# Performance work log

Hardware: AMD Instinct MI355X
Metric: run time of the kernel (lower is better)

## Reference

```python
import jax, jax.numpy as jnp
import numpy as np

B, IN, H = 8192, 1024, 1024

def setup_inputs() -> dict:
    key = jax.random.key(0)
    ks = jax.random.split(key, 7)
    s_in = 1.0 / np.sqrt(IN)
    s_h = 1.0 / np.sqrt(H)
    return {
        "x": jax.random.normal(ks[0], (B, IN), jnp.float32),
        "h": jax.random.normal(ks[1], (B, H), jnp.float32),
        "c": jax.random.normal(ks[2], (B, H), jnp.float32),
        "Wx": jax.random.normal(ks[3], (4, H, IN), jnp.float32) * s_in,
        "bx": jax.random.normal(ks[4], (4, H), jnp.float32) * s_in,
        "Wh": jax.random.normal(ks[5], (4, H, H), jnp.float32) * s_h,
        "bh": jax.random.normal(ks[6], (4, H), jnp.float32) * s_h,
    }

def reference(x, h, c, Wx, bx, Wh, bh):
    # gate order along axis g: 0=i (input), 1=f (forget), 2=g (cell), 3=o (output)
    # two fused GEMMs over all 4 gates: [B,4,H]
    gates = (jnp.einsum('bi,goi->bgo', x, Wx)
             + jnp.einsum('bj,goj->bgo', h, Wh)
             + bx[None] + bh[None])
    i = jax.nn.sigmoid(gates[:, 0])
    f = jax.nn.sigmoid(gates[:, 1])
    g = jnp.tanh(gates[:, 2])
    o = jax.nn.sigmoid(gates[:, 3])
    c_next = f * c + i * g
    h_next = o * jnp.tanh(c_next)
    return (h_next, c_next)
```

## Files before the change

kernel.cpp:

```cpp
#include <hip/hip_runtime.h>
#include <hip/hip_bf16.h>
#include <cstdint>
#include <cstddef>


#define B_DIM   8192
#define IN_DIM  1024
#define H_DIM   1024
#define KTOT    2048
#define BK      64
#define KSTEPS  (KTOT / BK)

typedef __attribute__((ext_vector_type(8))) short  bf16x8;
typedef __attribute__((ext_vector_type(4))) float  f32x4;

__device__ __forceinline__ void gld_lds16(const void* g, void* l) {
    __builtin_amdgcn_global_load_lds(
        (const __attribute__((address_space(1))) void*)g,
        (__attribute__((address_space(3))) void*)l, 16, 0, 0);
}

__device__ __forceinline__ unsigned short f2bf(float f) {
    union { float f; unsigned u; } v; v.f = f;
    unsigned r = v.u + 0x7fffu + ((v.u >> 16) & 1u);
    return (unsigned short)(r >> 16);
}

__global__ __launch_bounds__(256) void pack_a(const float* __restrict__ x,
                                              const float* __restrict__ h,
                                              unsigned short* __restrict__ Acat) {
    int idx = blockIdx.x * 256 + threadIdx.x;
    int row = idx >> 8;
    int k0  = (idx & 255) * 8;
    const float* src = (k0 < IN_DIM) ? (x + (size_t)row * IN_DIM + k0)
                                     : (h + (size_t)row * H_DIM + (k0 - IN_DIM));
    f32x4 v0 = *(const f32x4*)src;
    f32x4 v1 = *(const f32x4*)(src + 4);
    unsigned short tmp[8];
#pragma unroll
    for (int j = 0; j < 4; ++j) tmp[j]     = f2bf(v0[j]);
#pragma unroll
    for (int j = 0; j < 4; ++j) tmp[4 + j] = f2bf(v1[j]);
    *(bf16x8*)(Acat + (size_t)idx * 8) = *(const bf16x8*)tmp;
}

__global__ __launch_bounds__(256) void pack_w(const float* __restrict__ Wx,
                                              const float* __restrict__ Wh,
                                              unsigned short* __restrict__ Wcat) {
    int idx = blockIdx.x * 256 + threadIdx.x;
    int n   = idx >> 8;
    int k0  = (idx & 255) * 8;
    int ob = n >> 7, g = (n >> 5) & 3, ol = n & 31;
    int o  = ob * 32 + ol;
    const float* src = (k0 < IN_DIM)
        ? (Wx + ((size_t)(g * H_DIM + o)) * IN_DIM + k0)
        : (Wh + ((size_t)(g * H_DIM + o)) * H_DIM + (k0 - IN_DIM));
    f32x4 v0 = *(const f32x4*)src;
    f32x4 v1 = *(const f32x4*)(src + 4);
    unsigned short tmp[8];
#pragma unroll
    for (int j = 0; j < 4; ++j) tmp[j]     = f2bf(v0[j]);
#pragma unroll
    for (int j = 0; j < 4; ++j) tmp[4 + j] = f2bf(v1[j]);
    *(bf16x8*)(Wcat + (size_t)idx * 8) = *(const bf16x8*)tmp;
}

__device__ __forceinline__ float sigmoidf_fast(float v) {
    return 1.0f / (1.0f + __expf(-v));
}

__global__ __launch_bounds__(256, 2) void lstm_gemm(
        const unsigned short* __restrict__ Acat,
        const unsigned short* __restrict__ Wcat,
        const float* __restrict__ c,
        const float* __restrict__ bx,
        const float* __restrict__ bh,
        float* __restrict__ outH,
        float* __restrict__ outC) {
    __shared__ __align__(16) char smem[32768];
    char* ldsA = smem;
    char* ldsB = smem + 16384;

    const int t    = threadIdx.x;
    const int lane = t & 63;
    const int wid  = t >> 6;
    const int nb   = blockIdx.x;
    const int mb   = blockIdx.y;
    const int m0   = mb * 128;
    const int n0r  = nb * 128;
    const int l15  = lane & 15;
    const int l4   = lane >> 4;

    f32x4 acc[2][8];
#pragma unroll
    for (int i = 0; i < 2; ++i)
#pragma unroll
        for (int j = 0; j < 8; ++j)
#pragma unroll
            for (int e = 0; e < 4; ++e) acc[i][j][e] = 0.0f;

    const char* Abase = (const char*)Acat;
    const char* Wbase = (const char*)Wcat;

    for (int kt = 0; kt < KSTEPS; ++kt) {
        __syncthreads();
        const int kb0 = kt * 128;
#pragma unroll
        for (int q = 0; q < 4; ++q) {
            int off  = q * 4096 + t * 16;
            int row  = off >> 7;
            int scol = (off & 127) ^ ((row & 7) << 4);
            gld_lds16(Abase + ((size_t)(m0 + row) * (KTOT * 2) + kb0 + scol), ldsA + off);
        }
#pragma unroll
        for (int q = 0; q < 4; ++q) {
            int off  = q * 4096 + t * 16;
            int row  = off >> 7;
            int scol = (off & 127) ^ ((row & 7) << 4);
            gld_lds16(Wbase + ((size_t)(n0r + row) * (KTOT * 2) + kb0 + scol), ldsB + off);
        }
        __syncthreads();

#pragma unroll
        for (int kk = 0; kk < 2; ++kk) {
            const int kb = kk * 64 + l4 * 16;
            bf16x8 a[2], b[8];
#pragma unroll
            for (int mf = 0; mf < 2; ++mf) {
                int row = wid * 32 + mf * 16 + l15;
                a[mf] = *(const bf16x8*)(ldsA + row * 128 + (kb ^ ((row & 7) << 4)));
            }
#pragma unroll
            for (int nf = 0; nf < 8; ++nf) {
                int row = nf * 16 + l15;
                b[nf] = *(const bf16x8*)(ldsB + row * 128 + (kb ^ ((row & 7) << 4)));
            }
#pragma unroll
            for (int mf = 0; mf < 2; ++mf)
#pragma unroll
                for (int nf = 0; nf < 8; ++nf)
                    acc[mf][nf] = __builtin_amdgcn_mfma_f32_16x16x32_bf16(
                        a[mf], b[nf], acc[mf][nf], 0, 0, 0);
        }
    }

#pragma unroll
    for (int hh = 0; hh < 2; ++hh) {
        const int col = nb * 32 + hh * 16 + l15;
        const float bi = bx[col]            + bh[col];
        const float bf = bx[1024 + col]     + bh[1024 + col];
        const float bg = bx[2048 + col]     + bh[2048 + col];
        const float bo = bx[3072 + col]     + bh[3072 + col];
#pragma unroll
        for (int mf = 0; mf < 2; ++mf) {
#pragma unroll
            for (int j = 0; j < 4; ++j) {
                const int row = m0 + wid * 32 + mf * 16 + l4 * 4 + j;
                const float iv = acc[mf][0 + hh][j] + bi;
                const float fv = acc[mf][2 + hh][j] + bf;
                const float gv = acc[mf][4 + hh][j] + bg;
                const float ov = acc[mf][6 + hh][j] + bo;
                const float ig = sigmoidf_fast(iv);
                const float fg = sigmoidf_fast(fv);
                const float gg = tanhf(gv);
                const float og = sigmoidf_fast(ov);
                const float cin = c[(size_t)row * H_DIM + col];
                const float cn  = fg * cin + ig * gg;
                const float hn  = og * tanhf(cn);
                outH[(size_t)row * H_DIM + col] = hn;
                outC[(size_t)row * H_DIM + col] = cn;
            }
        }
    }
}

extern "C" void kernel_launch(void* const* d_in, const int* in_sizes, int n_in,
                              void* d_out, int out_size, void* d_ws, size_t ws_size,
                              hipStream_t stream) {
    const float* x  = (const float*)d_in[0];
    const float* h  = (const float*)d_in[1];
    const float* c  = (const float*)d_in[2];
    const float* Wx = (const float*)d_in[3];
    const float* bx = (const float*)d_in[4];
    const float* Wh = (const float*)d_in[5];
    const float* bh = (const float*)d_in[6];
    float* out = (float*)d_out;

    unsigned short* Acat = (unsigned short*)d_ws;
    unsigned short* Wcat = Acat + (size_t)B_DIM * KTOT;

    hipLaunchKernelGGL(pack_a, dim3(8192), dim3(256), 0, stream, x, h, Acat);
    hipLaunchKernelGGL(pack_w, dim3(4096), dim3(256), 0, stream, Wx, Wh, Wcat);
    hipLaunchKernelGGL(lstm_gemm, dim3(32, 64), dim3(256), 0, stream,
                       Acat, Wcat, c, bx, bh,
                       out, out + (size_t)B_DIM * H_DIM);
}
```

Measured before the change: 336.3 us.

## Rewrite LSTM GEMM with 256x256 tiles, double-buffered LDS and phased MFMA schedule

Replaces the 128x128 single-buffer GEMM with a 512-thread, 256x256-tile kernel. It double-buffers LDS and interleaves global-to-LDS prefetch of the next tiles with MFMA phases, using explicit barriers, waitcnts and setprio. The two packing kernels are merged into one launch, with a new weight interleave to match 16-column gate groups. The kernel also adds block swizzling for L2 locality and an exp-based tanh. The exchange is 128KB of LDS per block and much more fragile hand scheduling, and the fast tanh loses accuracy at extreme inputs.

```diff
diff --git a/kernel.cpp b/kernel.cpp
--- a/kernel.cpp
+++ b/kernel.cpp
@@ -8,32 +8,52 @@
 #define IN_DIM  1024
 #define H_DIM   1024
 #define KTOT    2048
-#define BK      64
-#define KSTEPS  (KTOT / BK)
+#define KROW    4096
+#define NT      32
 
 typedef __attribute__((ext_vector_type(8))) short  bf16x8;
 typedef __attribute__((ext_vector_type(4))) float  f32x4;
 
-__device__ __forceinline__ void gld_lds16(const void* g, void* l) {
+static __device__ __forceinline__ void gld_lds16(const void* g, void* l) {
     __builtin_amdgcn_global_load_lds(
         (const __attribute__((address_space(1))) void*)g,
         (__attribute__((address_space(3))) void*)l, 16, 0, 0);
 }
 
-__device__ __forceinline__ unsigned short f2bf(float f) {
+static __device__ __forceinline__ unsigned short f2bf(float f) {
     union { float f; unsigned u; } v; v.f = f;
     unsigned r = v.u + 0x7fffu + ((v.u >> 16) & 1u);
     return (unsigned short)(r >> 16);
 }
 
-__global__ __launch_bounds__(256) void pack_a(const float* __restrict__ x,
-                                              const float* __restrict__ h,
-                                              unsigned short* __restrict__ Acat) {
-    int idx = blockIdx.x * 256 + threadIdx.x;
-    int row = idx >> 8;
-    int k0  = (idx & 255) * 8;
-    const float* src = (k0 < IN_DIM) ? (x + (size_t)row * IN_DIM + k0)
-                                     : (h + (size_t)row * H_DIM + (k0 - IN_DIM));
+__global__ __launch_bounds__(256) void pack_all(const float* __restrict__ x,
+                                                const float* __restrict__ h,
+                                                const float* __restrict__ Wx,
+                                                const float* __restrict__ Wh,
+                                                unsigned short* __restrict__ Acat,
+                                                unsigned short* __restrict__ Wcat) {
+    const int bid = blockIdx.x;
+    const float* src;
+    unsigned short* dst;
+    int idx;
+    if (bid < 8192) {
+        idx = bid * 256 + threadIdx.x;
+        int row = idx >> 8;
+        int k0  = (idx & 255) * 8;
+        src = (k0 < IN_DIM) ? (x + (size_t)row * IN_DIM + k0)
+                            : (h + (size_t)row * H_DIM + (k0 - IN_DIM));
+        dst = Acat + (size_t)idx * 8;
+    } else {
+        idx = (bid - 8192) * 256 + threadIdx.x;
+        int n  = idx >> 8;
+        int k0 = (idx & 255) * 8;
+        int ob64 = n >> 6, g = (n >> 4) & 3, ol = n & 15;
+        int o = ob64 * 16 + ol;
+        src = (k0 < IN_DIM)
+            ? (Wx + (size_t)(g * H_DIM + o) * IN_DIM + k0)
+            : (Wh + (size_t)(g * H_DIM + o) * H_DIM + (k0 - IN_DIM));
+        dst = Wcat + (size_t)idx * 8;
+    }
     f32x4 v0 = *(const f32x4*)src;
     f32x4 v1 = *(const f32x4*)(src + 4);
     unsigned short tmp[8];
@@ -41,35 +61,139 @@
     for (int j = 0; j < 4; ++j) tmp[j]     = f2bf(v0[j]);
 #pragma unroll
     for (int j = 0; j < 4; ++j) tmp[4 + j] = f2bf(v1[j]);
-    *(bf16x8*)(Acat + (size_t)idx * 8) = *(const bf16x8*)tmp;
-}
-
-__global__ __launch_bounds__(256) void pack_w(const float* __restrict__ Wx,
-                                              const float* __restrict__ Wh,
-                                              unsigned short* __restrict__ Wcat) {
-    int idx = blockIdx.x * 256 + threadIdx.x;
-    int n   = idx >> 8;
-    int k0  = (idx & 255) * 8;
-    int ob = n >> 7, g = (n >> 5) & 3, ol = n & 31;
-    int o  = ob * 32 + ol;
-    const float* src = (k0 < IN_DIM)
-        ? (Wx + ((size_t)(g * H_DIM + o)) * IN_DIM + k0)
-        : (Wh + ((size_t)(g * H_DIM + o)) * H_DIM + (k0 - IN_DIM));
-    f32x4 v0 = *(const f32x4*)src;
-    f32x4 v1 = *(const f32x4*)(src + 4);
-    unsigned short tmp[8];
-#pragma unroll
-    for (int j = 0; j < 4; ++j) tmp[j]     = f2bf(v0[j]);
-#pragma unroll
-    for (int j = 0; j < 4; ++j) tmp[4 + j] = f2bf(v1[j]);
-    *(bf16x8*)(Wcat + (size_t)idx * 8) = *(const bf16x8*)tmp;
-}
-
-__device__ __forceinline__ float sigmoidf_fast(float v) {
+    *(bf16x8*)dst = *(const bf16x8*)tmp;
+}
+
+static __device__ __forceinline__ void stageA(const char* Ab, char* lds,
+                                              int m0, int kb, int pass, int tid) {
+    int off  = pass * 8192 + tid * 16;
+    int rowp = off >> 7;
+    int scol = (off & 127) ^ ((rowp & 7) << 4);
+    int mh = rowp >> 7, wmr = (rowp >> 6) & 1, rr = rowp & 63;
+    int r  = wmr * 128 + mh * 64 + rr;
+    gld_lds16(Ab + (size_t)(m0 + r) * KROW + kb + scol, lds + off);
+}
+static __device__ __forceinline__ void stageB(const char* Wb, char* lds,
+                                              int n0r, int kb, int pass, int tid) {
+    int off  = pass * 8192 + tid * 16;
+    int rowp = off >> 7;
+    int scol = (off & 127) ^ ((rowp & 7) << 4);
+    gld_lds16(Wb + (size_t)(n0r + rowp) * KROW + kb + scol, lds + off);
+}
+
+static __device__ __forceinline__ bf16x8 ldA(const char* lds, int wm, int mf, int kk,
+                                             int l15, int l4) {
+    int rowp = (mf >> 2) * 128 + wm * 64 + (mf & 3) * 16 + l15;
+    int kb   = kk * 64 + l4 * 16;
+    return *(const bf16x8*)(lds + rowp * 128 + (kb ^ ((rowp & 7) << 4)));
+}
+static __device__ __forceinline__ bf16x8 ldB(const char* lds, int wn, int nf, int kk,
+                                             int l15, int l4) {
+    int rowp = wn * 64 + nf * 16 + l15;
+    int kb   = kk * 64 + l4 * 16;
+    return *(const bf16x8*)(lds + rowp * 128 + (kb ^ ((rowp & 7) << 4)));
+}
+
+static __device__ __forceinline__ void fence_mem() {
+    __builtin_amdgcn_sched_barrier(0);
+    asm volatile("" ::: "memory");
+}
+static __device__ __forceinline__ void phase_barrier() {
+    fence_mem();
+    __builtin_amdgcn_s_barrier();
+    fence_mem();
+}
+
+static __device__ __forceinline__ float sigmoid_fast(float v) {
     return 1.0f / (1.0f + __expf(-v));
 }
-
-__global__ __launch_bounds__(256, 2) void lstm_gemm(
+static __device__ __forceinline__ float tanh_fast(float v) {
+    return 1.0f - 2.0f / (1.0f + __expf(2.0f * v));
+}
+
+template<int CUR>
+static __device__ __forceinline__ void do_tile(
+        int t, const char* Ab, const char* Wb,
+        char* bufA0, char* bufB0, char* bufA1, char* bufB1,
+        f32x4 (&acc)[8][4], bf16x8 (&b)[4][2],
+        int m0, int n0r, int tid, int wm, int wn, int l15, int l4) {
+    char* cA = CUR ? bufA1 : bufA0;
+    char* cB = CUR ? bufB1 : bufB0;
+    char* oA = CUR ? bufA0 : bufA1;
+    char* oB = CUR ? bufB0 : bufB1;
+    const int  kb1 = (t + 1) * 128, kb2 = (t + 2) * 128;
+    const bool g1 = (t + 1) < NT, g2 = (t + 2) < NT;
+    bf16x8 a[4];
+
+#pragma unroll
+    for (int mf = 0; mf < 4; ++mf) a[mf] = ldA(cA, wm, mf, 0, l15, l4);
+#pragma unroll
+    for (int nf = 0; nf < 4; ++nf) b[nf][0] = ldB(cB, wn, nf, 0, l15, l4);
+    if (g1) { stageB(Wb, oB, n0r, kb1, 2, tid); stageB(Wb, oB, n0r, kb1, 3, tid); }
+    phase_barrier();
+    asm volatile("s_waitcnt lgkmcnt(0)" ::: "memory");
+    __builtin_amdgcn_sched_barrier(0);
+    __builtin_amdgcn_s_setprio(1);
+#pragma unroll
+    for (int mf = 0; mf < 4; ++mf)
+#pragma unroll
+        for (int nf = 0; nf < 4; ++nf)
+            acc[mf][nf] = __builtin_amdgcn_mfma_f32_16x16x32_bf16(a[mf], b[nf][0], acc[mf][nf], 0, 0, 0);
+    __builtin_amdgcn_s_setprio(0);
+    phase_barrier();
+
+#pragma unroll
+    for (int mf = 0; mf < 4; ++mf) a[mf] = ldA(cA, wm, mf, 1, l15, l4);
+#pragma unroll
+    for (int nf = 0; nf < 4; ++nf) b[nf][1] = ldB(cB, wn, nf, 1, l15, l4);
+    if (g1) { stageA(Ab, oA, m0, kb1, 2, tid); stageA(Ab, oA, m0, kb1, 3, tid); }
+    phase_barrier();
+    asm volatile("s_waitcnt lgkmcnt(0)" ::: "memory");
+    __builtin_amdgcn_sched_barrier(0);
+    __builtin_amdgcn_s_setprio(1);
+#pragma unroll
+    for (int mf = 0; mf < 4; ++mf)
+#pragma unroll
+        for (int nf = 0; nf < 4; ++nf)
+            acc[mf][nf] = __builtin_amdgcn_mfma_f32_16x16x32_bf16(a[mf], b[nf][1], acc[mf][nf], 0, 0, 0);
+    __builtin_amdgcn_s_setprio(0);
+    phase_barrier();
+
+#pragma unroll
+    for (int mf = 0; mf < 4; ++mf) a[mf] = ldA(cA, wm, 4 + mf, 0, l15, l4);
+    if (g2) { stageA(Ab, cA, m0, kb2, 0, tid); stageA(Ab, cA, m0, kb2, 1, tid); }
+    phase_barrier();
+    asm volatile("s_waitcnt lgkmcnt(0)" ::: "memory");
+    __builtin_amdgcn_sched_barrier(0);
+    __builtin_amdgcn_s_setprio(1);
+#pragma unroll
+    for (int mf = 0; mf < 4; ++mf)
+#pragma unroll
+        for (int nf = 0; nf < 4; ++nf)
+            acc[4 + mf][nf] = __builtin_amdgcn_mfma_f32_16x16x32_bf16(a[mf], b[nf][0], acc[4 + mf][nf], 0, 0, 0);
+    __builtin_amdgcn_s_setprio(0);
+    phase_barrier();
+
+#pragma unroll
+    for (int mf = 0; mf < 4; ++mf) a[mf] = ldA(cA, wm, 4 + mf, 1, l15, l4);
+    if (g2) { stageB(Wb, cB, n0r, kb2, 0, tid); stageB(Wb, cB, n0r, kb2, 1, tid); }
+    phase_barrier();
+    asm volatile("s_waitcnt lgkmcnt(0)" ::: "memory");
+    __builtin_amdgcn_sched_barrier(0);
+    __builtin_amdgcn_s_setprio(1);
+#pragma unroll
+    for (int mf = 0; mf < 4; ++mf)
+#pragma unroll
+        for (int nf = 0; nf < 4; ++nf)
+            acc[4 + mf][nf] = __builtin_amdgcn_mfma_f32_16x16x32_bf16(a[mf], b[nf][1], acc[4 + mf][nf], 0, 0, 0);
+    __builtin_amdgcn_s_setprio(0);
+    fence_mem();
+    if (g2) { asm volatile("s_waitcnt vmcnt(4)" ::: "memory"); }
+    else    { asm volatile("s_waitcnt vmcnt(0)" ::: "memory"); }
+    phase_barrier();
+}
+
+__global__ __launch_bounds__(512, 2) void lstm_gemm(
         const unsigned short* __restrict__ Acat,
         const unsigned short* __restrict__ Wcat,
         const float* __restrict__ c,
@@ -77,99 +201,79 @@
         const float* __restrict__ bh,
         float* __restrict__ outH,
         float* __restrict__ outC) {
-    __shared__ __align__(16) char smem[32768];
-    char* ldsA = smem;
-    char* ldsB = smem + 16384;
-
-    const int t    = threadIdx.x;
-    const int lane = t & 63;
-    const int wid  = t >> 6;
-    const int nb   = blockIdx.x;
-    const int mb   = blockIdx.y;
-    const int m0   = mb * 128;
-    const int n0r  = nb * 128;
+    __shared__ __align__(16) char smem[131072];
+    char* bufA0 = smem;
+    char* bufB0 = smem + 32768;
+    char* bufA1 = smem + 65536;
+    char* bufB1 = smem + 98304;
+
+    const int tid  = threadIdx.x;
+    const int lane = tid & 63;
+    const int wid  = tid >> 6;
+    const int wm   = wid >> 2;
+    const int wn   = wid & 3;
     const int l15  = lane & 15;
     const int l4   = lane >> 4;
 
-    f32x4 acc[2][8];
-#pragma unroll
-    for (int i = 0; i < 2; ++i)
-#pragma unroll
-        for (int j = 0; j < 8; ++j)
+    const int bid = blockIdx.x;
+    const int swz = (bid & 7) * 64 + (bid >> 3);
+    const int mb  = swz >> 4;
+    const int nb  = swz & 15;
+    const int m0  = mb * 256;
+    const int n0r = nb * 256;
+
+    const char* Ab = (const char*)Acat;
+    const char* Wb = (const char*)Wcat;
+
+    f32x4 acc[8][4];
+#pragma unroll
+    for (int i = 0; i < 8; ++i)
+#pragma unroll
+        for (int j = 0; j < 4; ++j)
 #pragma unroll
             for (int e = 0; e < 4; ++e) acc[i][j][e] = 0.0f;
-
-    const char* Abase = (const char*)Acat;
-    const char* Wbase = (const char*)Wcat;
-
-    for (int kt = 0; kt < KSTEPS; ++kt) {
-        __syncthreads();
-        const int kb0 = kt * 128;
-#pragma unroll
-        for (int q = 0; q < 4; ++q) {
-            int off  = q * 4096 + t * 16;
-            int row  = off >> 7;
-            int scol = (off & 127) ^ ((row & 7) << 4);
-            gld_lds16(Abase + ((size_t)(m0 + row) * (KTOT * 2) + kb0 + scol), ldsA + off);
-        }
-#pragma unroll
-        for (int q = 0; q < 4; ++q) {
-            int off  = q * 4096 + t * 16;
-            int row  = off >> 7;
-            int scol = (off & 127) ^ ((row & 7) << 4);
-            gld_lds16(Wbase + ((size_t)(n0r + row) * (KTOT * 2) + kb0 + scol), ldsB + off);
-        }
-        __syncthreads();
-
-#pragma unroll
-        for (int kk = 0; kk < 2; ++kk) {
-            const int kb = kk * 64 + l4 * 16;
-            bf16x8 a[2], b[8];
-#pragma unroll
-            for (int mf = 0; mf < 2; ++mf) {
-                int row = wid * 32 + mf * 16 + l15;
-                a[mf] = *(const bf16x8*)(ldsA + row * 128 + (kb ^ ((row & 7) << 4)));
-            }
-#pragma unroll
-            for (int nf = 0; nf < 8; ++nf) {
-                int row = nf * 16 + l15;
-                b[nf] = *(const bf16x8*)(ldsB + row * 128 + (kb ^ ((row & 7) << 4)));
-            }
-#pragma unroll
-            for (int mf = 0; mf < 2; ++mf)
-#pragma unroll
-                for (int nf = 0; nf < 8; ++nf)
-                    acc[mf][nf] = __builtin_amdgcn_mfma_f32_16x16x32_bf16(
-                        a[mf], b[nf], acc[mf][nf], 0, 0, 0);
-        }
+    bf16x8 b[4][2];
+
+#pragma unroll
+    for (int p = 0; p < 4; ++p) stageA(Ab, bufA0, m0, 0, p, tid);
+#pragma unroll
+    for (int p = 0; p < 4; ++p) stageB(Wb, bufB0, n0r, 0, p, tid);
+    stageA(Ab, bufA1, m0, 128, 0, tid);
+    stageA(Ab, bufA1, m0, 128, 1, tid);
+    stageB(Wb, bufB1, n0r, 128, 0, tid);
+    stageB(Wb, bufB1, n0r, 128, 1, tid);
+    fence_mem();
+    asm volatile("s_waitcnt vmcnt(4)" ::: "memory");
+    phase_barrier();
+
+    for (int tt = 0; tt < NT; tt += 2) {
+        do_tile<0>(tt,     Ab, Wb, bufA0, bufB0, bufA1, bufB1, acc, b, m0, n0r, tid, wm, wn, l15, l4);
+        do_tile<1>(tt + 1, Ab, Wb, bufA0, bufB0, bufA1, bufB1, acc, b, m0, n0r, tid, wm, wn, l15, l4);
     }
 
-#pragma unroll
-    for (int hh = 0; hh < 2; ++hh) {
-        const int col = nb * 32 + hh * 16 + l15;
-        const float bi = bx[col]            + bh[col];
-        const float bf = bx[1024 + col]     + bh[1024 + col];
-        const float bg = bx[2048 + col]     + bh[2048 + col];
-        const float bo = bx[3072 + col]     + bh[3072 + col];
-#pragma unroll
-        for (int mf = 0; mf < 2; ++mf) {
-#pragma unroll
-            for (int j = 0; j < 4; ++j) {
-                const int row = m0 + wid * 32 + mf * 16 + l4 * 4 + j;
-                const float iv = acc[mf][0 + hh][j] + bi;
-                const float fv = acc[mf][2 + hh][j] + bf;
-                const float gv = acc[mf][4 + hh][j] + bg;
-                const float ov = acc[mf][6 + hh][j] + bo;
-                const float ig = sigmoidf_fast(iv);
-                const float fg = sigmoidf_fast(fv);
-                const float gg = tanhf(gv);
-                const float og = sigmoidf_fast(ov);
-                const float cin = c[(size_t)row * H_DIM + col];
-                const float cn  = fg * cin + ig * gg;
-                const float hn  = og * tanhf(cn);
-                outH[(size_t)row * H_DIM + col] = hn;
-                outC[(size_t)row * H_DIM + col] = cn;
-            }
+    const int col = (nb * 4 + wn) * 16 + l15;
+    const float bi = bx[col]            + bh[col];
+    const float bf = bx[1024 + col]     + bh[1024 + col];
+    const float bg = bx[2048 + col]     + bh[2048 + col];
+    const float bo = bx[3072 + col]     + bh[3072 + col];
+#pragma unroll
+    for (int mf = 0; mf < 8; ++mf) {
+#pragma unroll
+        for (int j = 0; j < 4; ++j) {
+            const int row = m0 + wm * 128 + mf * 16 + l4 * 4 + j;
+            const float iv = acc[mf][0][j] + bi;
+            const float fv = acc[mf][1][j] + bf;
+            const float gv = acc[mf][2][j] + bg;
+            const float ov = acc[mf][3][j] + bo;
+            const float ig = sigmoid_fast(iv);
+            const float fg = sigmoid_fast(fv);
+            const float gg = tanh_fast(gv);
+            const float og = sigmoid_fast(ov);
+            const float cin = c[(size_t)row * H_DIM + col];
+            const float cn  = fg * cin + ig * gg;
+            const float hn  = og * tanh_fast(cn);
+            outH[(size_t)row * H_DIM + col] = hn;
+            outC[(size_t)row * H_DIM + col] = cn;
         }
     }
 }
@@ -189,9 +293,8 @@
     unsigned short* Acat = (unsigned short*)d_ws;
     unsigned short* Wcat = Acat + (size_t)B_DIM * KTOT;
 
-    hipLaunchKernelGGL(pack_a, dim3(8192), dim3(256), 0, stream, x, h, Acat);
-    hipLaunchKernelGGL(pack_w, dim3(4096), dim3(256), 0, stream, Wx, Wh, Wcat);
-    hipLaunchKernelGGL(lstm_gemm, dim3(32, 64), dim3(256), 0, stream,
+    hipLaunchKernelGGL(pack_all, dim3(12288), dim3(256), 0, stream, x, h, Wx, Wh, Acat, Wcat);
+    hipLaunchKernelGGL(lstm_gemm, dim3(512), dim3(512), 0, stream,
                        Acat, Wcat, c, bx, bh,
                        out, out + (size_t)B_DIM * H_DIM);
 }
```

Measured after the change: 300.2 us. -10.8%, faster.
